# Optimization experiments

Hardware: AMD Instinct MI355X
Metric: run time of the kernel (lower is better)

The kernel has to match this reference:

```python
import jax, jax.numpy as jnp
import numpy as np

DIM = 1024
DIM_HEAD = 64
HEADS = 8
MULT = 4
ATTN_INNER = HEADS * DIM_HEAD            # 512
FF_INNER = MULT * DIM                    # 4096
FUSED = ATTN_INNER + DIM_HEAD + DIM_HEAD + 2 * FF_INNER  # 8832


def setup_inputs() -> dict:
    key = jax.random.key(0)
    ks = jax.random.split(key, 5)
    x = jax.random.normal(ks[0], (2, 2048, DIM), dtype=jnp.float32)
    gamma = jnp.ones((DIM,), dtype=jnp.float32)
    # Linear weights stored as [in, out]
    w_fused = jax.random.normal(ks[1], (DIM, FUSED), dtype=jnp.float32) * (DIM ** -0.5)
    w_attn_out = jax.random.normal(ks[2], (ATTN_INNER, DIM), dtype=jnp.float32) * (ATTN_INNER ** -0.5)
    w_ff_out = jax.random.normal(ks[3], (FF_INNER, DIM), dtype=jnp.float32) * (FF_INNER ** -0.5)
    return {"x": x, "gamma": gamma, "w_fused": w_fused,
            "w_attn_out": w_attn_out, "w_ff_out": w_ff_out}


def _forward(x, gamma, w_fused, w_attn_out, w_ff_out):
    b, n, d = x.shape
    # LayerNorm (beta buffer is zeros)
    mu = jnp.mean(x, axis=-1, keepdims=True)
    var = jnp.mean(jnp.square(x - mu), axis=-1, keepdims=True)
    xn = (x - mu) * jax.lax.rsqrt(var + 1e-5) * gamma
    # fused QKV + FF projection
    proj = jnp.einsum('bnd,df->bnf', xn, w_fused)
    q = proj[..., :ATTN_INNER]
    k = proj[..., ATTN_INNER:ATTN_INNER + DIM_HEAD]
    v = proj[..., ATTN_INNER + DIM_HEAD:ATTN_INNER + 2 * DIM_HEAD]
    ff = proj[..., ATTN_INNER + 2 * DIM_HEAD:]
    # multi-query attention: single shared K/V head of width DIM_HEAD
    q = q.reshape(b, n, HEADS, DIM_HEAD).transpose(0, 2, 1, 3) * (DIM_HEAD ** -0.5)
    sim = jnp.einsum('bhid,bjd->bhij', q, k)
    attn = jax.nn.softmax(sim, axis=-1)
    out = jnp.einsum('bhij,bjd->bhid', attn, v)
    out = out.transpose(0, 2, 1, 3).reshape(b, n, ATTN_INNER)
    attn_out = jnp.einsum('bna,ad->bnd', out, w_attn_out)
    # parallel SwiGLU FF: chunk -> (x_part, gate); silu(gate)*x_part
    ff_x, gate = ff[..., :FF_INNER], ff[..., FF_INNER:]
    ff_out = jnp.einsum('bnf,fd->bnd', jax.nn.silu(gate) * ff_x, w_ff_out)
    return attn_out + ff_out


def reference(x, gamma, w_fused, w_attn_out, w_ff_out):
    return _forward(x, gamma, w_fused, w_attn_out, w_ff_out)
```

## Files before the change

### kernel.cpp

```cpp
#include <hip/hip_runtime.h>
#include <hip/hip_bf16.h>
#include <stdint.h>

#define DIM     1024
#define SEQ     2048
#define NTOK    4096
#define HEADS   8
#define DH      64
#define AINNER  512
#define FFI     4096
#define FUSED   8832
#define HCOLS   4608

typedef __attribute__((ext_vector_type(8))) short short8;
typedef __attribute__((ext_vector_type(4))) short short4v;
typedef __attribute__((ext_vector_type(4))) float f32x4;

__device__ __forceinline__ short f2bf(float f) {
  union { float f; uint32_t u; } v; v.f = f;
  uint32_t r = v.u + 0x7fffu + ((v.u >> 16) & 1u);
  return (short)(r >> 16);
}
__device__ __forceinline__ float bf2f(short s) {
  union { uint32_t u; float f; } v; v.u = ((uint32_t)(uint16_t)s) << 16;
  return v.f;
}
__device__ __forceinline__ void g2l16(const void* g, void* l) {
  __builtin_amdgcn_global_load_lds((const __attribute__((address_space(1))) void*)g,
                                   (__attribute__((address_space(3))) void*)l, 16, 0, 0);
}

#define PH_W4 asm volatile("s_waitcnt vmcnt(4)\ns_barrier" ::: "memory")
#define PH_W2 asm volatile("s_waitcnt vmcnt(2)\ns_barrier" ::: "memory")
#define PH_W0 asm volatile("s_waitcnt vmcnt(0)\ns_barrier" ::: "memory")
#define PH_B  asm volatile("s_barrier" ::: "memory")

__global__ __launch_bounds__(256) void k_transpose_wf(const float* __restrict__ src,
                                                      short* __restrict__ dst) {
  __shared__ short tile[32][33];
  int c0 = blockIdx.x * 32;
  int r0 = blockIdx.y * 32;
  int tx = threadIdx.x & 31, ty = threadIdx.x >> 5;
#pragma unroll
  for (int i = 0; i < 32; i += 8)
    tile[ty + i][tx] = f2bf(src[(size_t)(r0 + ty + i) * FUSED + c0 + tx]);
  __syncthreads();
#pragma unroll
  for (int i = 0; i < 32; i += 8)
    dst[(size_t)(c0 + ty + i) * DIM + r0 + tx] = tile[tx][ty + i];
}

__global__ __launch_bounds__(256) void k_transpose_w2(const float* __restrict__ wao,
                                                      const float* __restrict__ wfo,
                                                      short* __restrict__ dst) {
  __shared__ short tile[32][33];
  int c0 = blockIdx.x * 32;
  int r0 = blockIdx.y * 32;
  int tx = threadIdx.x & 31, ty = threadIdx.x >> 5;
#pragma unroll
  for (int i = 0; i < 32; i += 8) {
    int r = r0 + ty + i;
    float v = (r < AINNER) ? wao[(size_t)r * DIM + c0 + tx]
                           : wfo[(size_t)(r - AINNER) * DIM + c0 + tx];
    tile[ty + i][tx] = f2bf(v);
  }
  __syncthreads();
#pragma unroll
  for (int i = 0; i < 32; i += 8)
    dst[(size_t)(c0 + ty + i) * HCOLS + r0 + tx] = tile[tx][ty + i];
}

__global__ __launch_bounds__(256) void k_ln(const float* __restrict__ x,
                                            const float* __restrict__ gamma,
                                            short* __restrict__ xn) {
  int row = blockIdx.x;
  int t = threadIdx.x;
  const float4* xr = (const float4*)(x + (size_t)row * DIM);
  float4 v = xr[t];
  float s = v.x + v.y + v.z + v.w;
  float s2 = v.x * v.x + v.y * v.y + v.z * v.z + v.w * v.w;
#pragma unroll
  for (int m = 1; m < 64; m <<= 1) { s += __shfl_xor(s, m); s2 += __shfl_xor(s2, m); }
  __shared__ float red[8];
  int w = t >> 6;
  if ((t & 63) == 0) { red[w] = s; red[4 + w] = s2; }
  __syncthreads();
  s = red[0] + red[1] + red[2] + red[3];
  s2 = red[4] + red[5] + red[6] + red[7];
  float mu = s * (1.f / DIM);
  float rs = rsqrtf(s2 * (1.f / DIM) - mu * mu + 1e-5f);
  const float4* g4 = (const float4*)gamma;
  float4 g = g4[t];
  short4v o;
  o.x = f2bf((v.x - mu) * rs * g.x);
  o.y = f2bf((v.y - mu) * rs * g.y);
  o.z = f2bf((v.z - mu) * rs * g.z);
  o.w = f2bf((v.w - mu) * rs * g.w);
  ((short4v*)(xn + (size_t)row * DIM))[t] = o;
}

__global__ __launch_bounds__(512, 2) void p1(const short* __restrict__ A,
                                             const short* __restrict__ Bt,
                                             short* __restrict__ qb,
                                             short* __restrict__ kbf,
                                             short* __restrict__ vtb,
                                             short* __restrict__ H) {
  extern __shared__ __align__(16) short S[];
  int tid = threadIdx.x, l = tid & 63, w = tid >> 6;
  int hw = blockIdx.y * 37 + blockIdx.x;
  int tile = (hw & 7) * 74 + (hw >> 3);
  int c = tile / 74, j = tile % 74;
  bool fused = j < 64;
  int bx, by;
  if (fused) { int f = c * 64 + j; by = f >> 5; bx = f & 31; }
  else       { int q = c * 10 + (j - 64); by = q / 5; bx = 32 + q % 5; }
  int mBase = by * 256;
  int b0row = fused ? (640 + bx * 128) : ((bx - 32) * 128);
  int b1row = 4736 + bx * 128;

  int srow = w * 8 + (l >> 3);
  int cs = (l & 7) ^ (l >> 3);
  const short* Ag = A + (size_t)(mBase + srow) * DIM + cs * 8;
  const short* Bg0 = Bt + (size_t)(b0row + srow) * DIM + cs * 8;
  const short* Bg1 = Bt + (size_t)(b1row + srow) * DIM + cs * 8;
  int dsto = w * 512 + l * 8;

#define STG_A0(kt, db) { _Pragma("unroll") for (int i = 0; i < 2; ++i) \
    g2l16(Ag + (size_t)(i * 64) * DIM + (kt) * 64, S + (db) * 16384 + i * 4096 + dsto); }
#define STG_A1(kt, db) { _Pragma("unroll") for (int i = 2; i < 4; ++i) \
    g2l16(Ag + (size_t)(i * 64) * DIM + (kt) * 64, S + (db) * 16384 + i * 4096 + dsto); }
#define STG_B0(kt, db) { _Pragma("unroll") for (int i = 0; i < 2; ++i) \
    g2l16(Bg0 + (size_t)(i * 64) * DIM + (kt) * 64, S + 32768 + (db) * 16384 + i * 4096 + dsto); }
#define STG_B1(kt, db) { _Pragma("unroll") for (int i = 0; i < 2; ++i) \
    g2l16(Bg1 + (size_t)(i * 64) * DIM + (kt) * 64, S + 32768 + (db) * 16384 + 8192 + i * 4096 + dsto); }

  const int NT = DIM / 64;
  int c0 = l & 15, kg = l >> 4, cx = l & 7;
  int ch0 = (kg ^ cx) * 8, ch1 = ((4 + kg) ^ cx) * 8;
  int r0 = (l >> 4) * 4;
  f32x4 zero = {0.f, 0.f, 0.f, 0.f};

  if (!fused) {
    STG_A0(0, 0); STG_A1(0, 0); STG_B0(0, 0);
    int wm = w >> 2, wn = w & 3;
    f32x4 acc[8][2];
#pragma unroll
    for (int m = 0; m < 8; ++m) { acc[m][0] = zero; acc[m][1] = zero; }
    for (int kt = 0; kt < NT; ++kt) {
      int db = kt & 1, dbn = db ^ 1;
      PH_W0;
      if (kt + 1 < NT) { STG_A0(kt + 1, dbn); STG_A1(kt + 1, dbn); STG_B0(kt + 1, dbn); }
      const short* Ab = S + db * 16384;
      const short* Bb = S + 32768 + db * 16384;
#pragma unroll
      for (int kkh = 0; kkh < 2; ++kkh) {
        int ch8 = kkh ? ch1 : ch0;
        short8 b0 = *(const short8*)(Bb + (wn * 32 + c0) * 64 + ch8);
        short8 b1 = *(const short8*)(Bb + (wn * 32 + 16 + c0) * 64 + ch8);
        __builtin_amdgcn_s_setprio(1);
#pragma unroll
        for (int m = 0; m < 8; ++m) {
          short8 a = *(const short8*)(Ab + (wm * 128 + m * 16 + c0) * 64 + ch8);
          acc[m][0] = __builtin_amdgcn_mfma_f32_16x16x32_bf16(a, b0, acc[m][0], 0, 0, 0);
          acc[m][1] = __builtin_amdgcn_mfma_f32_16x16x32_bf16(a, b1, acc[m][1], 0, 0, 0);
        }
        __builtin_amdgcn_s_setprio(0);
      }
    }
#pragma unroll
    for (int m = 0; m < 8; ++m)
#pragma unroll
      for (int n = 0; n < 2; ++n)
#pragma unroll
        for (int r = 0; r < 4; ++r) {
          float val = acc[m][n][r];
          int row = mBase + wm * 128 + m * 16 + r0 + r;
          int col = (bx - 32) * 128 + wn * 32 + n * 16 + c0;
          if (col < AINNER)
            qb[(size_t)row * AINNER + col] = f2bf(val);
          else if (col < AINNER + DH)
            kbf[(size_t)row * DH + (col - AINNER)] = f2bf(val);
          else
            vtb[((size_t)(row >> 11) * DH + (col - AINNER - DH)) * SEQ +
                (row & (SEQ - 1))] = f2bf(val);
        }
    return;
  }

  STG_A0(0, 0); STG_B0(0, 0); STG_B1(0, 0); STG_A1(0, 0);
  int ra = (w >> 2) * 64, rb = (w & 3) * 32;
  f32x4 acc[2][2][4][2];
#pragma unroll
  for (int a = 0; a < 2; ++a)
#pragma unroll
    for (int b = 0; b < 2; ++b)
#pragma unroll
      for (int m = 0; m < 4; ++m)
#pragma unroll
        for (int n = 0; n < 2; ++n) acc[a][b][m][n] = zero;

  for (int kt = 0; kt < NT; ++kt) {
    int db = kt & 1, dbn = db ^ 1;
    bool st = kt + 1 < NT;
    const short* Ab = S + db * 16384;
    const short* Bb = S + 32768 + db * 16384;
    short8 a1[4][2], a2[4][2], bF[2][2], bG[2][2];
    PH_W4;
#pragma unroll
    for (int m = 0; m < 4; ++m) {
      a1[m][0] = *(const short8*)(Ab + (ra + m * 16 + c0) * 64 + ch0);
      a1[m][1] = *(const short8*)(Ab + (ra + m * 16 + c0) * 64 + ch1);
    }
#pragma unroll
    for (int n = 0; n < 2; ++n) {
      bF[n][0] = *(const short8*)(Bb + (rb + n * 16 + c0) * 64 + ch0);
      bF[n][1] = *(const short8*)(Bb + (rb + n * 16 + c0) * 64 + ch1);
    }
    if (st) STG_A0(kt + 1, dbn);
    PH_B;
    __builtin_amdgcn_s_setprio(1);
#pragma unroll
    for (int m = 0; m < 4; ++m)
#pragma unroll
      for (int n = 0; n < 2; ++n) {
        acc[0][0][m][n] = __builtin_amdgcn_mfma_f32_16x16x32_bf16(a1[m][0], bF[n][0], acc[0][0][m][n], 0, 0, 0);
        acc[0][0][m][n] = __builtin_amdgcn_mfma_f32_16x16x32_bf16(a1[m][1], bF[n][1], acc[0][0][m][n], 0, 0, 0);
      }
    __builtin_amdgcn_s_setprio(0);
    if (st) PH_W4; else PH_W2;
#pragma unroll
    for (int n = 0; n < 2; ++n) {
      bG[n][0] = *(const short8*)(Bb + 8192 + (rb + n * 16 + c0) * 64 + ch0);
      bG[n][1] = *(const short8*)(Bb + 8192 + (rb + n * 16 + c0) * 64 + ch1);
    }
    if (st) STG_B0(kt + 1, dbn);
    PH_B;
    __builtin_amdgcn_s_setprio(1);
#pragma unroll
    for (int m = 0; m < 4; ++m)
#pragma unroll
      for (int n = 0; n < 2; ++n) {
        acc[0][1][m][n] = __builtin_amdgcn_mfma_f32_16x16x32_bf16(a1[m][0], bG[n][0], acc[0][1][m][n], 0, 0, 0);
        acc[0][1][m][n] = __builtin_amdgcn_mfma_f32_16x16x32_bf16(a1[m][1], bG[n][1], acc[0][1][m][n], 0, 0, 0);
      }
    __builtin_amdgcn_s_setprio(0);
    if (st) PH_W4; else PH_W0;
#pragma unroll
    for (int m = 0; m < 4; ++m) {
      a2[m][0] = *(const short8*)(Ab + 8192 + (ra + m * 16 + c0) * 64 + ch0);
      a2[m][1] = *(const short8*)(Ab + 8192 + (ra + m * 16 + c0) * 64 + ch1);
    }
    if (st) STG_B1(kt + 1, dbn);
    PH_B;
    __builtin_amdgcn_s_setprio(1);
#pragma unroll
    for (int m = 0; m < 4; ++m)
#pragma unroll
      for (int n = 0; n < 2; ++n) {
        acc[1][1][m][n] = __builtin_amdgcn_mfma_f32_16x16x32_bf16(a2[m][0], bG[n][0], acc[1][1][m][n], 0, 0, 0);
        acc[1][1][m][n] = __builtin_amdgcn_mfma_f32_16x16x32_bf16(a2[m][1], bG[n][1], acc[1][1][m][n], 0, 0, 0);
      }
    __builtin_amdgcn_s_setprio(0);
    if (st) STG_A1(kt + 1, dbn);
    __builtin_amdgcn_s_setprio(1);
#pragma unroll
    for (int m = 0; m < 4; ++m)
#pragma unroll
      for (int n = 0; n < 2; ++n) {
        acc[1][0][m][n] = __builtin_amdgcn_mfma_f32_16x16x32_bf16(a2[m][0], bF[n][0], acc[1][0][m][n], 0, 0, 0);
        acc[1][0][m][n] = __builtin_amdgcn_mfma_f32_16x16x32_bf16(a2[m][1], bF[n][1], acc[1][0][m][n], 0, 0, 0);
      }
    __builtin_amdgcn_s_setprio(0);
  }
#undef STG_A0
#undef STG_A1
#undef STG_B0
#undef STG_B1

#pragma unroll
  for (int a = 0; a < 2; ++a)
#pragma unroll
    for (int m = 0; m < 4; ++m)
#pragma unroll
      for (int n = 0; n < 2; ++n)
#pragma unroll
        for (int r = 0; r < 4; ++r) {
          int row = mBase + a * 128 + ra + m * 16 + r0 + r;
          int col = bx * 128 + rb + n * 16 + c0;
          float g = acc[a][1][m][n][r];
          float sg = g / (1.f + __expf(-g));
          H[(size_t)row * HCOLS + AINNER + col] = f2bf(sg * acc[a][0][m][n][r]);
        }
}

__global__ __launch_bounds__(512, 2) void gemm_s(const short* __restrict__ A,
                                                 const short* __restrict__ Bt,
                                                 short* __restrict__ part) {
  extern __shared__ __align__(16) short S[];
  int tid = threadIdx.x, l = tid & 63, w = tid >> 6;
  int hw = (blockIdx.z * 16 + blockIdx.y) * 4 + blockIdx.x;
  int tile = (hw & 7) * 32 + (hw >> 3);
  int bx = tile & 3, by = (tile >> 2) & 15, bz = tile >> 6;
  int mBase = by * 256, nBase = bx * 256;
  int kOff = bz * 1152;

  int srow = w * 8 + (l >> 3);
  int cs = (l & 7) ^ (l >> 3);
  const short* Ag = A + (size_t)(mBase + srow) * HCOLS + kOff + cs * 8;
  const short* Bg = Bt + (size_t)(nBase + srow) * HCOLS + kOff + cs * 8;
  int dsto = w * 512 + l * 8;

#define SG_A0(kt, db) { _Pragma("unroll") for (int i = 0; i < 2; ++i) \
    g2l16(Ag + (size_t)(i * 64) * HCOLS + (kt) * 64, S + (db) * 16384 + i * 4096 + dsto); }
#define SG_A1(kt, db) { _Pragma("unroll") for (int i = 2; i < 4; ++i) \
    g2l16(Ag + (size_t)(i * 64) * HCOLS + (kt) * 64, S + (db) * 16384 + i * 4096 + dsto); }
#define SG_B0(kt, db) { _Pragma("unroll") for (int i = 0; i < 2; ++i) \
    g2l16(Bg + (size_t)(i * 64) * HCOLS + (kt) * 64, S + 32768 + (db) * 16384 + i * 4096 + dsto); }
#define SG_B1(kt, db) { _Pragma("unroll") for (int i = 2; i < 4; ++i) \
    g2l16(Bg + (size_t)(i * 64) * HCOLS + (kt) * 64, S + 32768 + (db) * 16384 + i * 4096 + dsto); }

  const int NT = 18;
  SG_A0(0, 0); SG_B0(0, 0); SG_B1(0, 0); SG_A1(0, 0);

  int c0 = l & 15, kg = l >> 4, cx = l & 7;
  int ch0 = (kg ^ cx) * 8, ch1 = ((4 + kg) ^ cx) * 8;
  int ra = (w >> 2) * 64, rb = (w & 3) * 32;
  f32x4 zero = {0.f, 0.f, 0.f, 0.f};
  f32x4 acc[2][2][4][2];
#pragma unroll
  for (int a = 0; a < 2; ++a)
#pragma unroll
    for (int b = 0; b < 2; ++b)
#pragma unroll
      for (int m = 0; m < 4; ++m)
#pragma unroll
        for (int n = 0; n < 2; ++n) acc[a][b][m][n] = zero;

  for (int kt = 0; kt < NT; ++kt) {
    int db = kt & 1, dbn = db ^ 1;
    bool st = kt + 1 < NT;
    const short* Ab = S + db * 16384;
    const short* Bb = S + 32768 + db * 16384;
    short8 a1[4][2], a2[4][2], bF[2][2], bG[2][2];
    PH_W4;
#pragma unroll
    for (int m = 0; m < 4; ++m) {
      a1[m][0] = *(const short8*)(Ab + (ra + m * 16 + c0) * 64 + ch0);
      a1[m][1] = *(const short8*)(Ab + (ra + m * 16 + c0) * 64 + ch1);
    }
#pragma unroll
    for (int n = 0; n < 2; ++n) {
      bF[n][0] = *(const short8*)(Bb + (rb + n * 16 + c0) * 64 + ch0);
      bF[n][1] = *(const short8*)(Bb + (rb + n * 16 + c0) * 64 + ch1);
    }
    if (st) SG_A0(kt + 1, dbn);
    PH_B;
    __builtin_amdgcn_s_setprio(1);
#pragma unroll
    for (int m = 0; m < 4; ++m)
#pragma unroll
      for (int n = 0; n < 2; ++n) {
        acc[0][0][m][n] = __builtin_amdgcn_mfma_f32_16x16x32_bf16(a1[m][0], bF[n][0], acc[0][0][m][n], 0, 0, 0);
        acc[0][0][m][n] = __builtin_amdgcn_mfma_f32_16x16x32_bf16(a1[m][1], bF[n][1], acc[0][0][m][n], 0, 0, 0);
      }
    __builtin_amdgcn_s_setprio(0);
    if (st) PH_W4; else PH_W2;
#pragma unroll
    for (int n = 0; n < 2; ++n) {
      bG[n][0] = *(const short8*)(Bb + 8192 + (rb + n * 16 + c0) * 64 + ch0);
      bG[n][1] = *(const short8*)(Bb + 8192 + (rb + n * 16 + c0) * 64 + ch1);
    }
    if (st) SG_B0(kt + 1, dbn);
    PH_B;
    __builtin_amdgcn_s_setprio(1);
#pragma unroll
    for (int m = 0; m < 4; ++m)
#pragma unroll
      for (int n = 0; n < 2; ++n) {
        acc[0][1][m][n] = __builtin_amdgcn_mfma_f32_16x16x32_bf16(a1[m][0], bG[n][0], acc[0][1][m][n], 0, 0, 0);
        acc[0][1][m][n] = __builtin_amdgcn_mfma_f32_16x16x32_bf16(a1[m][1], bG[n][1], acc[0][1][m][n], 0, 0, 0);
      }
    __builtin_amdgcn_s_setprio(0);
    if (st) PH_W4; else PH_W0;
#pragma unroll
    for (int m = 0; m < 4; ++m) {
      a2[m][0] = *(const short8*)(Ab + 8192 + (ra + m * 16 + c0) * 64 + ch0);
      a2[m][1] = *(const short8*)(Ab + 8192 + (ra + m * 16 + c0) * 64 + ch1);
    }
    if (st) SG_B1(kt + 1, dbn);
    PH_B;
    __builtin_amdgcn_s_setprio(1);
#pragma unroll
    for (int m = 0; m < 4; ++m)
#pragma unroll
      for (int n = 0; n < 2; ++n) {
        acc[1][1][m][n] = __builtin_amdgcn_mfma_f32_16x16x32_bf16(a2[m][0], bG[n][0], acc[1][1][m][n], 0, 0, 0);
        acc[1][1][m][n] = __builtin_amdgcn_mfma_f32_16x16x32_bf16(a2[m][1], bG[n][1], acc[1][1][m][n], 0, 0, 0);
      }
    __builtin_amdgcn_s_setprio(0);
    if (st) SG_A1(kt + 1, dbn);
    __builtin_amdgcn_s_setprio(1);
#pragma unroll
    for (int m = 0; m < 4; ++m)
#pragma unroll
      for (int n = 0; n < 2; ++n) {
        acc[1][0][m][n] = __builtin_amdgcn_mfma_f32_16x16x32_bf16(a2[m][0], bF[n][0], acc[1][0][m][n], 0, 0, 0);
        acc[1][0][m][n] = __builtin_amdgcn_mfma_f32_16x16x32_bf16(a2[m][1], bF[n][1], acc[1][0][m][n], 0, 0, 0);
      }
    __builtin_amdgcn_s_setprio(0);
  }
#undef SG_A0
#undef SG_A1
#undef SG_B0
#undef SG_B1

  int r0 = (l >> 4) * 4;
#pragma unroll
  for (int a = 0; a < 2; ++a)
#pragma unroll
    for (int b = 0; b < 2; ++b)
#pragma unroll
      for (int m = 0; m < 4; ++m)
#pragma unroll
        for (int n = 0; n < 2; ++n)
#pragma unroll
          for (int r = 0; r < 4; ++r) {
            int row = mBase + a * 128 + ra + m * 16 + r0 + r;
            int col = nBase + b * 128 + rb + n * 16 + c0;
            part[(size_t)bz * (NTOK * DIM) + (size_t)row * DIM + col] = f2bf(acc[a][b][m][n][r]);
          }
}

__global__ __launch_bounds__(256) void k_red(const short* __restrict__ part,
                                             float* __restrict__ out) {
  int i = (blockIdx.x * 256 + threadIdx.x) * 8;
  float s[8] = {0.f, 0.f, 0.f, 0.f, 0.f, 0.f, 0.f, 0.f};
#pragma unroll
  for (int ks = 0; ks < 4; ++ks) {
    short8 v = *(const short8*)(part + (size_t)ks * (NTOK * DIM) + i);
#pragma unroll
    for (int jj = 0; jj < 8; ++jj) s[jj] += bf2f(v[jj]);
  }
  float4 lo = {s[0], s[1], s[2], s[3]};
  float4 hi = {s[4], s[5], s[6], s[7]};
  *(float4*)(out + i) = lo;
  *(float4*)(out + i + 4) = hi;
}

__global__ __launch_bounds__(256) void k_attn(const short* __restrict__ qb,
                                              const short* __restrict__ kb,
                                              const short* __restrict__ vt,
                                              short* __restrict__ H) {
  __shared__ __align__(16) short Qs[64 * 64];
  __shared__ __align__(16) short Ks[128 * 64];
  __shared__ __align__(16) short Vs[64 * 128];
  __shared__ __align__(16) short Ps[4][16 * 128];
  int t = threadIdx.x, l = t & 63, w = t >> 6;
  int qt = blockIdx.x, bh = blockIdx.y;
  int b = bh >> 3, h = bh & 7;
  int q0 = qt * 64;

  int srow = w * 8 + (l >> 3);
  int schunk = (l & 7) ^ (l >> 3);
  {
    const short* Qg = qb + (size_t)(b * SEQ + q0 + srow) * AINNER + h * DH + schunk * 8;
    short* qs = Qs + w * 512 + l * 8;
#pragma unroll
    for (int i = 0; i < 2; ++i) g2l16(Qg + (size_t)(i * 32) * AINNER, qs + i * 2048);
  }
  const short* Kg = kb + (size_t)(b * SEQ + srow) * DH + schunk * 8;
  short* ksl = Ks + w * 512 + l * 8;
  int vrow = w * 4 + (l >> 4);
  int vchunk = (l & 15) ^ (vrow & 7);
  const short* Vg = vt + (size_t)b * DH * SEQ + (size_t)vrow * SEQ + vchunk * 8;
  short* vsl = Vs + w * 512 + l * 8;

#pragma unroll
  for (int i = 0; i < 4; ++i) {
    g2l16(Kg + (size_t)(i * 32) * DH, ksl + i * 2048);
    g2l16(Vg + (size_t)(i * 16) * SEQ, vsl + i * 2048);
  }

  float m_run[4], l_run[4];
  f32x4 zero = {0.f, 0.f, 0.f, 0.f};
  f32x4 Oacc[4];
#pragma unroll
  for (int r = 0; r < 4; ++r) { m_run[r] = -1e30f; l_run[r] = 0.f; }
#pragma unroll
  for (int n = 0; n < 4; ++n) Oacc[n] = zero;

  int c0 = l & 15, kg = l >> 4, cx = l & 7;
  short* pw = Ps[w];

  for (int kv0 = 0; kv0 < SEQ; kv0 += 128) {
    asm volatile("s_waitcnt vmcnt(0)\ns_barrier" ::: "memory");

    f32x4 sacc[8];
#pragma unroll
    for (int n = 0; n < 8; ++n) sacc[n] = zero;
#pragma unroll
    for (int kk = 0; kk < 2; ++kk) {
      int rr = w * 16 + c0;
      short8 aq = *(const short8*)(Qs + rr * 64 + ((kk * 4 + kg) ^ cx) * 8);
#pragma unroll
      for (int n = 0; n < 8; ++n) {
        int kr = n * 16 + c0;
        short8 bk = *(const short8*)(Ks + kr * 64 + ((kk * 4 + kg) ^ cx) * 8);
        sacc[n] = __builtin_amdgcn_mfma_f32_16x16x32_bf16(aq, bk, sacc[n], 0, 0, 0);
      }
    }
#pragma unroll
    for (int r = 0; r < 4; ++r) {
      float mx = -1e30f;
#pragma unroll
      for (int n = 0; n < 8; ++n) {
        sacc[n][r] *= 0.125f;
        mx = fmaxf(mx, sacc[n][r]);
      }
#pragma unroll
      for (int msk = 1; msk < 16; msk <<= 1) mx = fmaxf(mx, __shfl_xor(mx, msk));
      float nm = fmaxf(m_run[r], mx);
      float corr = __expf(m_run[r] - nm);
      m_run[r] = nm;
      float rs = 0.f;
#pragma unroll
      for (int n = 0; n < 8; ++n) {
        float p = __expf(sacc[n][r] - nm);
        sacc[n][r] = p;
        rs += p;
      }
#pragma unroll
      for (int msk = 1; msk < 16; msk <<= 1) rs += __shfl_xor(rs, msk);
      l_run[r] = l_run[r] * corr + rs;
      Oacc[0][r] *= corr; Oacc[1][r] *= corr; Oacc[2][r] *= corr; Oacc[3][r] *= corr;
    }
#pragma unroll
    for (int n = 0; n < 8; ++n)
#pragma unroll
      for (int r = 0; r < 4; ++r) {
        int pr = (l >> 4) * 4 + r;
        int pc = n * 16 + c0;
        pw[pr * 128 + ((pc >> 3) ^ (pr & 7)) * 8 + (pc & 7)] = f2bf(sacc[n][r]);
      }
    asm volatile("s_waitcnt lgkmcnt(0)" ::: "memory");
#pragma unroll
    for (int kk = 0; kk < 4; ++kk) {
      int pr = c0;
      short8 ap = *(const short8*)(pw + pr * 128 + ((kk * 4 + kg) ^ cx) * 8);
#pragma unroll
      for (int n = 0; n < 4; ++n) {
        int vr = n * 16 + c0;
        short8 bv = *(const short8*)(Vs + vr * 128 + ((kk * 4 + kg) ^ (vr & 7)) * 8);
        Oacc[n] = __builtin_amdgcn_mfma_f32_16x16x32_bf16(ap, bv, Oacc[n], 0, 0, 0);
      }
    }
    __syncthreads();
    int nx = kv0 + 128;
    if (nx < SEQ) {
#pragma unroll
      for (int i = 0; i < 4; ++i) {
        g2l16(Kg + (size_t)(nx + i * 32) * DH, ksl + i * 2048);
        g2l16(Vg + nx + (size_t)(i * 16) * SEQ, vsl + i * 2048);
      }
    }
  }
#pragma unroll
  for (int r = 0; r < 4; ++r) {
    float inv = 1.f / l_run[r];
    int row = b * SEQ + q0 + w * 16 + (l >> 4) * 4 + r;
#pragma unroll
    for (int n = 0; n < 4; ++n) {
      int col = h * DH + n * 16 + c0;
      H[(size_t)row * HCOLS + col] = f2bf(Oacc[n][r] * inv);
    }
  }
}

extern "C" void kernel_launch(void* const* d_in, const int* in_sizes, int n_in,
                              void* d_out, int out_size, void* d_ws, size_t ws_size,
                              hipStream_t stream) {
  const float* x     = (const float*)d_in[0];
  const float* gamma = (const float*)d_in[1];
  const float* w_f   = (const float*)d_in[2];
  const float* w_ao  = (const float*)d_in[3];
  const float* w_fo  = (const float*)d_in[4];
  float* out = (float*)d_out;

  char* ws = (char*)d_ws;
  size_t o = 0;
  short* WtF = (short*)(ws + o); o += (size_t)FUSED * DIM * 2;
  short* Wt2 = (short*)(ws + o); o += (size_t)DIM * HCOLS * 2;
  short* xn  = (short*)(ws + o); o += (size_t)NTOK * DIM * 2;
  short* qb  = (short*)(ws + o); o += (size_t)NTOK * AINNER * 2;
  short* kbf = (short*)(ws + o); o += (size_t)NTOK * DH * 2;
  short* vtb = (short*)(ws + o); o += (size_t)NTOK * DH * 2;
  short* H   = (short*)(ws + o); o += (size_t)NTOK * HCOLS * 2;
  short* part = (short*)(ws + o);

  k_transpose_wf<<<dim3(FUSED / 32, DIM / 32), 256, 0, stream>>>(w_f, WtF);
  k_transpose_w2<<<dim3(DIM / 32, HCOLS / 32), 256, 0, stream>>>(w_ao, w_fo, Wt2);
  k_ln<<<NTOK, 256, 0, stream>>>(x, gamma, xn);
  p1<<<dim3(37, 16), 512, 131072, stream>>>(xn, WtF, qb, kbf, vtb, H);
  k_attn<<<dim3(32, 16), 256, 0, stream>>>(qb, kbf, vtb, H);
  gemm_s<<<dim3(4, 16, 4), 512, 131072, stream>>>(H, Wt2, part);
  k_red<<<NTOK * DIM / 2048, 256, 0, stream>>>(part, out);
}
```

Measured before the change: 211.1 us.

## Merge prep kernels into one launch and shrink p1 K-tile to raise occupancy

Merges the two weight transposes and the LayerNorm into a single k_prep launch dispatched by block index, removing two kernel launches. The p1 projection GEMM drops its K-tile from 64 to 32, halving LDS to 64 KB and raising launch bounds to allow 4 blocks per CU. It also replaces the hand-staged multi-phase pipeline in the fused SwiGLU path with a simpler double-buffered loop. Smaller K-tiles mean twice as many barriers and more frequent global-to-LDS waits, and the extra blocks per CU raise register pressure.

Measured after the change: 583.3 us. 2.76x slower.

```diff
diff --git a/kernel.cpp b/kernel.cpp
--- a/kernel.cpp
+++ b/kernel.cpp
@@ -35,71 +35,72 @@
 #define PH_W0 asm volatile("s_waitcnt vmcnt(0)\ns_barrier" ::: "memory")
 #define PH_B  asm volatile("s_barrier" ::: "memory")
 
-__global__ __launch_bounds__(256) void k_transpose_wf(const float* __restrict__ src,
-                                                      short* __restrict__ dst) {
+__global__ __launch_bounds__(256) void k_prep(const float* __restrict__ wf,
+                                              const float* __restrict__ wao,
+                                              const float* __restrict__ wfo,
+                                              const float* __restrict__ x,
+                                              const float* __restrict__ gamma,
+                                              short* __restrict__ WtF,
+                                              short* __restrict__ Wt2,
+                                              short* __restrict__ xn) {
   __shared__ short tile[32][33];
-  int c0 = blockIdx.x * 32;
-  int r0 = blockIdx.y * 32;
-  int tx = threadIdx.x & 31, ty = threadIdx.x >> 5;
-#pragma unroll
-  for (int i = 0; i < 32; i += 8)
-    tile[ty + i][tx] = f2bf(src[(size_t)(r0 + ty + i) * FUSED + c0 + tx]);
-  __syncthreads();
-#pragma unroll
-  for (int i = 0; i < 32; i += 8)
-    dst[(size_t)(c0 + ty + i) * DIM + r0 + tx] = tile[tx][ty + i];
-}
-
-__global__ __launch_bounds__(256) void k_transpose_w2(const float* __restrict__ wao,
-                                                      const float* __restrict__ wfo,
-                                                      short* __restrict__ dst) {
-  __shared__ short tile[32][33];
-  int c0 = blockIdx.x * 32;
-  int r0 = blockIdx.y * 32;
-  int tx = threadIdx.x & 31, ty = threadIdx.x >> 5;
-#pragma unroll
-  for (int i = 0; i < 32; i += 8) {
-    int r = r0 + ty + i;
-    float v = (r < AINNER) ? wao[(size_t)r * DIM + c0 + tx]
-                           : wfo[(size_t)(r - AINNER) * DIM + c0 + tx];
-    tile[ty + i][tx] = f2bf(v);
-  }
-  __syncthreads();
-#pragma unroll
-  for (int i = 0; i < 32; i += 8)
-    dst[(size_t)(c0 + ty + i) * HCOLS + r0 + tx] = tile[tx][ty + i];
-}
-
-__global__ __launch_bounds__(256) void k_ln(const float* __restrict__ x,
-                                            const float* __restrict__ gamma,
-                                            short* __restrict__ xn) {
-  int row = blockIdx.x;
-  int t = threadIdx.x;
-  const float4* xr = (const float4*)(x + (size_t)row * DIM);
-  float4 v = xr[t];
-  float s = v.x + v.y + v.z + v.w;
-  float s2 = v.x * v.x + v.y * v.y + v.z * v.z + v.w * v.w;
-#pragma unroll
-  for (int m = 1; m < 64; m <<= 1) { s += __shfl_xor(s, m); s2 += __shfl_xor(s2, m); }
   __shared__ float red[8];
-  int w = t >> 6;
-  if ((t & 63) == 0) { red[w] = s; red[4 + w] = s2; }
-  __syncthreads();
-  s = red[0] + red[1] + red[2] + red[3];
-  s2 = red[4] + red[5] + red[6] + red[7];
-  float mu = s * (1.f / DIM);
-  float rs = rsqrtf(s2 * (1.f / DIM) - mu * mu + 1e-5f);
-  const float4* g4 = (const float4*)gamma;
-  float4 g = g4[t];
-  short4v o;
-  o.x = f2bf((v.x - mu) * rs * g.x);
-  o.y = f2bf((v.y - mu) * rs * g.y);
-  o.z = f2bf((v.z - mu) * rs * g.z);
-  o.w = f2bf((v.w - mu) * rs * g.w);
-  ((short4v*)(xn + (size_t)row * DIM))[t] = o;
-}
-
-__global__ __launch_bounds__(512, 2) void p1(const short* __restrict__ A,
+  int bid = blockIdx.x;
+  if (bid < 8832) {
+    int bx = bid % 276, by = bid / 276;
+    int c0 = bx * 32, r0 = by * 32;
+    int tx = threadIdx.x & 31, ty = threadIdx.x >> 5;
+#pragma unroll
+    for (int i = 0; i < 32; i += 8)
+      tile[ty + i][tx] = f2bf(wf[(size_t)(r0 + ty + i) * FUSED + c0 + tx]);
+    __syncthreads();
+#pragma unroll
+    for (int i = 0; i < 32; i += 8)
+      WtF[(size_t)(c0 + ty + i) * DIM + r0 + tx] = tile[tx][ty + i];
+  } else if (bid < 13440) {
+    int idx = bid - 8832;
+    int bx = idx & 31, by = idx >> 5;
+    int c0 = bx * 32, r0 = by * 32;
+    int tx = threadIdx.x & 31, ty = threadIdx.x >> 5;
+#pragma unroll
+    for (int i = 0; i < 32; i += 8) {
+      int r = r0 + ty + i;
+      float v = (r < AINNER) ? wao[(size_t)r * DIM + c0 + tx]
+                             : wfo[(size_t)(r - AINNER) * DIM + c0 + tx];
+      tile[ty + i][tx] = f2bf(v);
+    }
+    __syncthreads();
+#pragma unroll
+    for (int i = 0; i < 32; i += 8)
+      Wt2[(size_t)(c0 + ty + i) * HCOLS + r0 + tx] = tile[tx][ty + i];
+  } else {
+    int row = bid - 13440;
+    int t = threadIdx.x;
+    const float4* xr = (const float4*)(x + (size_t)row * DIM);
+    float4 v = xr[t];
+    float s = v.x + v.y + v.z + v.w;
+    float s2 = v.x * v.x + v.y * v.y + v.z * v.z + v.w * v.w;
+#pragma unroll
+    for (int m = 1; m < 64; m <<= 1) { s += __shfl_xor(s, m); s2 += __shfl_xor(s2, m); }
+    int w = t >> 6;
+    if ((t & 63) == 0) { red[w] = s; red[4 + w] = s2; }
+    __syncthreads();
+    s = red[0] + red[1] + red[2] + red[3];
+    s2 = red[4] + red[5] + red[6] + red[7];
+    float mu = s * (1.f / DIM);
+    float rs = rsqrtf(s2 * (1.f / DIM) - mu * mu + 1e-5f);
+    const float4* g4 = (const float4*)gamma;
+    float4 g = g4[t];
+    short4v o;
+    o.x = f2bf((v.x - mu) * rs * g.x);
+    o.y = f2bf((v.y - mu) * rs * g.y);
+    o.z = f2bf((v.z - mu) * rs * g.z);
+    o.w = f2bf((v.w - mu) * rs * g.w);
+    ((short4v*)(xn + (size_t)row * DIM))[t] = o;
+  }
+}
+
+__global__ __launch_bounds__(512, 4) void p1(const short* __restrict__ A,
                                              const short* __restrict__ Bt,
                                              short* __restrict__ qb,
                                              short* __restrict__ kbf,
@@ -118,179 +119,143 @@
   int b0row = fused ? (640 + bx * 128) : ((bx - 32) * 128);
   int b1row = 4736 + bx * 128;
 
-  int srow = w * 8 + (l >> 3);
-  int cs = (l & 7) ^ (l >> 3);
-  const short* Ag = A + (size_t)(mBase + srow) * DIM + cs * 8;
+  int srow = w * 16 + (l >> 2);
+  int cs = (l & 3) ^ ((l >> 2) & 3);
+  const short* Ag0 = A + (size_t)(mBase + srow) * DIM + cs * 8;
+  const short* Ag1 = Ag0 + (size_t)128 * DIM;
   const short* Bg0 = Bt + (size_t)(b0row + srow) * DIM + cs * 8;
   const short* Bg1 = Bt + (size_t)(b1row + srow) * DIM + cs * 8;
   int dsto = w * 512 + l * 8;
 
-#define STG_A0(kt, db) { _Pragma("unroll") for (int i = 0; i < 2; ++i) \
-    g2l16(Ag + (size_t)(i * 64) * DIM + (kt) * 64, S + (db) * 16384 + i * 4096 + dsto); }
-#define STG_A1(kt, db) { _Pragma("unroll") for (int i = 2; i < 4; ++i) \
-    g2l16(Ag + (size_t)(i * 64) * DIM + (kt) * 64, S + (db) * 16384 + i * 4096 + dsto); }
-#define STG_B0(kt, db) { _Pragma("unroll") for (int i = 0; i < 2; ++i) \
-    g2l16(Bg0 + (size_t)(i * 64) * DIM + (kt) * 64, S + 32768 + (db) * 16384 + i * 4096 + dsto); }
-#define STG_B1(kt, db) { _Pragma("unroll") for (int i = 0; i < 2; ++i) \
-    g2l16(Bg1 + (size_t)(i * 64) * DIM + (kt) * 64, S + 32768 + (db) * 16384 + 8192 + i * 4096 + dsto); }
-
-  const int NT = DIM / 64;
-  int c0 = l & 15, kg = l >> 4, cx = l & 7;
-  int ch0 = (kg ^ cx) * 8, ch1 = ((4 + kg) ^ cx) * 8;
+  const int NT = DIM / 32;
+  int c0 = l & 15, kg = l >> 4;
+  int jc = (kg ^ (c0 & 3)) * 8;
   int r0 = (l >> 4) * 4;
+  int ra = (w >> 2) * 64, rb = (w & 3) * 32;
   f32x4 zero = {0.f, 0.f, 0.f, 0.f};
 
-  if (!fused) {
-    STG_A0(0, 0); STG_A1(0, 0); STG_B0(0, 0);
-    int wm = w >> 2, wn = w & 3;
-    f32x4 acc[8][2];
-#pragma unroll
-    for (int m = 0; m < 8; ++m) { acc[m][0] = zero; acc[m][1] = zero; }
+#define P1S_F(kt, db)                                                          \
+  {                                                                            \
+    g2l16(Ag0 + (kt) * 32, S + (db) * 8192 + dsto);                            \
+    g2l16(Ag1 + (kt) * 32, S + (db) * 8192 + 4096 + dsto);                     \
+    g2l16(Bg0 + (kt) * 32, S + 16384 + (db) * 8192 + dsto);                    \
+    g2l16(Bg1 + (kt) * 32, S + 16384 + (db) * 8192 + 4096 + dsto);             \
+  }
+#define P1S_Q(kt, db)                                                          \
+  {                                                                            \
+    g2l16(Ag0 + (kt) * 32, S + (db) * 8192 + dsto);                            \
+    g2l16(Ag1 + (kt) * 32, S + (db) * 8192 + 4096 + dsto);                     \
+    g2l16(Bg0 + (kt) * 32, S + 16384 + (db) * 8192 + dsto);                    \
+  }
+
+  if (fused) {
+    P1S_F(0, 0);
+    f32x4 accF[2][4][2], accG[2][4][2];
+#pragma unroll
+    for (int a = 0; a < 2; ++a)
+#pragma unroll
+      for (int m = 0; m < 4; ++m)
+#pragma unroll
+        for (int n = 0; n < 2; ++n) { accF[a][m][n] = zero; accG[a][m][n] = zero; }
     for (int kt = 0; kt < NT; ++kt) {
       int db = kt & 1, dbn = db ^ 1;
       PH_W0;
-      if (kt + 1 < NT) { STG_A0(kt + 1, dbn); STG_A1(kt + 1, dbn); STG_B0(kt + 1, dbn); }
-      const short* Ab = S + db * 16384;
-      const short* Bb = S + 32768 + db * 16384;
-#pragma unroll
-      for (int kkh = 0; kkh < 2; ++kkh) {
-        int ch8 = kkh ? ch1 : ch0;
-        short8 b0 = *(const short8*)(Bb + (wn * 32 + c0) * 64 + ch8);
-        short8 b1 = *(const short8*)(Bb + (wn * 32 + 16 + c0) * 64 + ch8);
+      if (kt + 1 < NT) P1S_F(kt + 1, dbn);
+      const short* Ab = S + db * 8192;
+      const short* Bb = S + 16384 + db * 8192;
+      short8 bF[2], bG[2];
+#pragma unroll
+      for (int n = 0; n < 2; ++n) {
+        bF[n] = *(const short8*)(Bb + (rb + n * 16 + c0) * 32 + jc);
+        bG[n] = *(const short8*)(Bb + (4096 + (rb + n * 16 + c0) * 32) + jc);
+      }
+#pragma unroll
+      for (int a = 0; a < 2; ++a) {
+        short8 av[4];
+#pragma unroll
+        for (int m = 0; m < 4; ++m)
+          av[m] = *(const short8*)(Ab + (a * 128 + ra + m * 16 + c0) * 32 + jc);
         __builtin_amdgcn_s_setprio(1);
 #pragma unroll
-        for (int m = 0; m < 8; ++m) {
-          short8 a = *(const short8*)(Ab + (wm * 128 + m * 16 + c0) * 64 + ch8);
-          acc[m][0] = __builtin_amdgcn_mfma_f32_16x16x32_bf16(a, b0, acc[m][0], 0, 0, 0);
-          acc[m][1] = __builtin_amdgcn_mfma_f32_16x16x32_bf16(a, b1, acc[m][1], 0, 0, 0);
-        }
+        for (int m = 0; m < 4; ++m)
+#pragma unroll
+          for (int n = 0; n < 2; ++n) {
+            accF[a][m][n] = __builtin_amdgcn_mfma_f32_16x16x32_bf16(av[m], bF[n], accF[a][m][n], 0, 0, 0);
+            accG[a][m][n] = __builtin_amdgcn_mfma_f32_16x16x32_bf16(av[m], bG[n], accG[a][m][n], 0, 0, 0);
+          }
         __builtin_amdgcn_s_setprio(0);
       }
     }
 #pragma unroll
-    for (int m = 0; m < 8; ++m)
+    for (int a = 0; a < 2; ++a)
+#pragma unroll
+      for (int m = 0; m < 4; ++m)
+#pragma unroll
+        for (int n = 0; n < 2; ++n)
+#pragma unroll
+          for (int r = 0; r < 4; ++r) {
+            int row = mBase + a * 128 + ra + m * 16 + r0 + r;
+            int col = bx * 128 + rb + n * 16 + c0;
+            float g = accG[a][m][n][r];
+            float sg = g / (1.f + __expf(-g));
+            H[(size_t)row * HCOLS + AINNER + col] = f2bf(sg * accF[a][m][n][r]);
+          }
+  } else {
+    P1S_Q(0, 0);
+    f32x4 acc[2][4][2];
+#pragma unroll
+    for (int a = 0; a < 2; ++a)
+#pragma unroll
+      for (int m = 0; m < 4; ++m)
+#pragma unroll
+        for (int n = 0; n < 2; ++n) acc[a][m][n] = zero;
+    for (int kt = 0; kt < NT; ++kt) {
+      int db = kt & 1, dbn = db ^ 1;
+      PH_W0;
+      if (kt + 1 < NT) P1S_Q(kt + 1, dbn);
+      const short* Ab = S + db * 8192;
+      const short* Bb = S + 16384 + db * 8192;
+      short8 bF[2];
 #pragma unroll
       for (int n = 0; n < 2; ++n)
-#pragma unroll
-        for (int r = 0; r < 4; ++r) {
-          float val = acc[m][n][r];
-          int row = mBase + wm * 128 + m * 16 + r0 + r;
-          int col = (bx - 32) * 128 + wn * 32 + n * 16 + c0;
-          if (col < AINNER)
-            qb[(size_t)row * AINNER + col] = f2bf(val);
-          else if (col < AINNER + DH)
-            kbf[(size_t)row * DH + (col - AINNER)] = f2bf(val);
-          else
-            vtb[((size_t)(row >> 11) * DH + (col - AINNER - DH)) * SEQ +
-                (row & (SEQ - 1))] = f2bf(val);
-        }
-    return;
-  }
-
-  STG_A0(0, 0); STG_B0(0, 0); STG_B1(0, 0); STG_A1(0, 0);
-  int ra = (w >> 2) * 64, rb = (w & 3) * 32;
-  f32x4 acc[2][2][4][2];
-#pragma unroll
-  for (int a = 0; a < 2; ++a)
-#pragma unroll
-    for (int b = 0; b < 2; ++b)
+        bF[n] = *(const short8*)(Bb + (rb + n * 16 + c0) * 32 + jc);
+#pragma unroll
+      for (int a = 0; a < 2; ++a) {
+        short8 av[4];
+#pragma unroll
+        for (int m = 0; m < 4; ++m)
+          av[m] = *(const short8*)(Ab + (a * 128 + ra + m * 16 + c0) * 32 + jc);
+        __builtin_amdgcn_s_setprio(1);
+#pragma unroll
+        for (int m = 0; m < 4; ++m)
+#pragma unroll
+          for (int n = 0; n < 2; ++n)
+            acc[a][m][n] = __builtin_amdgcn_mfma_f32_16x16x32_bf16(av[m], bF[n], acc[a][m][n], 0, 0, 0);
+        __builtin_amdgcn_s_setprio(0);
+      }
+    }
+#pragma unroll
+    for (int a = 0; a < 2; ++a)
 #pragma unroll
       for (int m = 0; m < 4; ++m)
 #pragma unroll
-        for (int n = 0; n < 2; ++n) acc[a][b][m][n] = zero;
-
-  for (int kt = 0; kt < NT; ++kt) {
-    int db = kt & 1, dbn = db ^ 1;
-    bool st = kt + 1 < NT;
-    const short* Ab = S + db * 16384;
-    const short* Bb = S + 32768 + db * 16384;
-    short8 a1[4][2], a2[4][2], bF[2][2], bG[2][2];
-    PH_W4;
-#pragma unroll
-    for (int m = 0; m < 4; ++m) {
-      a1[m][0] = *(const short8*)(Ab + (ra + m * 16 + c0) * 64 + ch0);
-      a1[m][1] = *(const short8*)(Ab + (ra + m * 16 + c0) * 64 + ch1);
-    }
-#pragma unroll
-    for (int n = 0; n < 2; ++n) {
-      bF[n][0] = *(const short8*)(Bb + (rb + n * 16 + c0) * 64 + ch0);
-      bF[n][1] = *(const short8*)(Bb + (rb + n * 16 + c0) * 64 + ch1);
-    }
-    if (st) STG_A0(kt + 1, dbn);
-    PH_B;
-    __builtin_amdgcn_s_setprio(1);
-#pragma unroll
-    for (int m = 0; m < 4; ++m)
-#pragma unroll
-      for (int n = 0; n < 2; ++n) {
-        acc[0][0][m][n] = __builtin_amdgcn_mfma_f32_16x16x32_bf16(a1[m][0], bF[n][0], acc[0][0][m][n], 0, 0, 0);
-        acc[0][0][m][n] = __builtin_amdgcn_mfma_f32_16x16x32_bf16(a1[m][1], bF[n][1], acc[0][0][m][n], 0, 0, 0);
-      }
-    __builtin_amdgcn_s_setprio(0);
-    if (st) PH_W4; else PH_W2;
-#pragma unroll
-    for (int n = 0; n < 2; ++n) {
-      bG[n][0] = *(const short8*)(Bb + 8192 + (rb + n * 16 + c0) * 64 + ch0);
-      bG[n][1] = *(const short8*)(Bb + 8192 + (rb + n * 16 + c0) * 64 + ch1);
-    }
-    if (st) STG_B0(kt + 1, dbn);
-    PH_B;
-    __builtin_amdgcn_s_setprio(1);
-#pragma unroll
-    for (int m = 0; m < 4; ++m)
-#pragma unroll
-      for (int n = 0; n < 2; ++n) {
-        acc[0][1][m][n] = __builtin_amdgcn_mfma_f32_16x16x32_bf16(a1[m][0], bG[n][0], acc[0][1][m][n], 0, 0, 0);
-        acc[0][1][m][n] = __builtin_amdgcn_mfma_f32_16x16x32_bf16(a1[m][1], bG[n][1], acc[0][1][m][n], 0, 0, 0);
-      }
-    __builtin_amdgcn_s_setprio(0);
-    if (st) PH_W4; else PH_W0;
-#pragma unroll
-    for (int m = 0; m < 4; ++m) {
-      a2[m][0] = *(const short8*)(Ab + 8192 + (ra + m * 16 + c0) * 64 + ch0);
-      a2[m][1] = *(const short8*)(Ab + 8192 + (ra + m * 16 + c0) * 64 + ch1);
-    }
-    if (st) STG_B1(kt + 1, dbn);
-    PH_B;
-    __builtin_amdgcn_s_setprio(1);
-#pragma unroll
-    for (int m = 0; m < 4; ++m)
-#pragma unroll
-      for (int n = 0; n < 2; ++n) {
-        acc[1][1][m][n] = __builtin_amdgcn_mfma_f32_16x16x32_bf16(a2[m][0], bG[n][0], acc[1][1][m][n], 0, 0, 0);
-        acc[1][1][m][n] = __builtin_amdgcn_mfma_f32_16x16x32_bf16(a2[m][1], bG[n][1], acc[1][1][m][n], 0, 0, 0);
-      }
-    __builtin_amdgcn_s_setprio(0);
-    if (st) STG_A1(kt + 1, dbn);
-    __builtin_amdgcn_s_setprio(1);
-#pragma unroll
-    for (int m = 0; m < 4; ++m)
-#pragma unroll
-      for (int n = 0; n < 2; ++n) {
-        acc[1][0][m][n] = __builtin_amdgcn_mfma_f32_16x16x32_bf16(a2[m][0], bF[n][0], acc[1][0][m][n], 0, 0, 0);
-        acc[1][0][m][n] = __builtin_amdgcn_mfma_f32_16x16x32_bf16(a2[m][1], bF[n][1], acc[1][0][m][n], 0, 0, 0);
-      }
-    __builtin_amdgcn_s_setprio(0);
-  }
-#undef STG_A0
-#undef STG_A1
-#undef STG_B0
-#undef STG_B1
-
-#pragma unroll
-  for (int a = 0; a < 2; ++a)
-#pragma unroll
-    for (int m = 0; m < 4; ++m)
-#pragma unroll
-      for (int n = 0; n < 2; ++n)
-#pragma unroll
-        for (int r = 0; r < 4; ++r) {
-          int row = mBase + a * 128 + ra + m * 16 + r0 + r;
-          int col = bx * 128 + rb + n * 16 + c0;
-          float g = acc[a][1][m][n][r];
-          float sg = g / (1.f + __expf(-g));
-          H[(size_t)row * HCOLS + AINNER + col] = f2bf(sg * acc[a][0][m][n][r]);
-        }
+        for (int n = 0; n < 2; ++n)
+#pragma unroll
+          for (int r = 0; r < 4; ++r) {
+            float val = acc[a][m][n][r];
+            int row = mBase + a * 128 + ra + m * 16 + r0 + r;
+            int col = (bx - 32) * 128 + rb + n * 16 + c0;
+            if (col < AINNER)
+              qb[(size_t)row * AINNER + col] = f2bf(val);
+            else if (col < AINNER + DH)
+              kbf[(size_t)row * DH + (col - AINNER)] = f2bf(val);
+            else
+              vtb[((size_t)(row >> 11) * DH + (col - AINNER - DH)) * SEQ +
+                  (row & (SEQ - 1))] = f2bf(val);
+          }
+  }
+#undef P1S_F
+#undef P1S_Q
 }
 
 __global__ __launch_bounds__(512, 2) void gemm_s(const short* __restrict__ A,
@@ -597,10 +562,8 @@
   short* H   = (short*)(ws + o); o += (size_t)NTOK * HCOLS * 2;
   short* part = (short*)(ws + o);
 
-  k_transpose_wf<<<dim3(FUSED / 32, DIM / 32), 256, 0, stream>>>(w_f, WtF);
-  k_transpose_w2<<<dim3(DIM / 32, HCOLS / 32), 256, 0, stream>>>(w_ao, w_fo, Wt2);
-  k_ln<<<NTOK, 256, 0, stream>>>(x, gamma, xn);
-  p1<<<dim3(37, 16), 512, 131072, stream>>>(xn, WtF, qb, kbf, vtb, H);
+  k_prep<<<17536, 256, 0, stream>>>(w_f, w_ao, w_fo, x, gamma, WtF, Wt2, xn);
+  p1<<<dim3(37, 16), 512, 65536, stream>>>(xn, WtF, qb, kbf, vtb, H);
   k_attn<<<dim3(32, 16), 256, 0, stream>>>(qb, kbf, vtb, H);
   gemm_s<<<dim3(4, 16, 4), 512, 131072, stream>>>(H, Wt2, part);
   k_red<<<NTOK * DIM / 2048, 256, 0, stream>>>(part, out);
```
